# Kernel optimization log

Hardware: AMD Instinct MI355X
Metric: run time of the kernel (lower is better)

## Reference

```python
import jax, jax.numpy as jnp
import numpy as np

B, S, DM, H = 2, 4096, 512, 8
DEPTH = DM // H


def setup_inputs() -> dict:
    key = jax.random.key(0)
    ks = jax.random.split(key, 12)
    scale = 1.0 / np.sqrt(DM)
    return {
        "q": jax.random.normal(ks[0], (B, S, DM), jnp.float32),
        "k": jax.random.normal(ks[1], (B, S, DM), jnp.float32),
        "v": jax.random.normal(ks[2], (B, S, DM), jnp.float32),
        # padding-style mask: 1.0 = masked position, 0.0 = attend
        "mask": jax.random.bernoulli(ks[3], 0.1, (B, 1, 1, S)).astype(jnp.float32),
        "Wq": jax.random.normal(ks[4], (DM, DM), jnp.float32) * scale,
        "bq": jnp.zeros((DM,), jnp.float32),
        "Wk": jax.random.normal(ks[5], (DM, DM), jnp.float32) * scale,
        "bk": jnp.zeros((DM,), jnp.float32),
        "Wv": jax.random.normal(ks[6], (DM, DM), jnp.float32) * scale,
        "bv": jnp.zeros((DM,), jnp.float32),
        "Wo": jax.random.normal(ks[7], (DM, DM), jnp.float32) * scale,
        "bo": jnp.zeros((DM,), jnp.float32),
    }


def _split_heads(x):
    # [B, S, DM] -> [B, H, S, DEPTH]
    b, s, _ = x.shape
    return x.reshape(b, s, H, DEPTH).transpose(0, 2, 1, 3)


def reference(q, k, v, mask, Wq, bq, Wk, bk, Wv, bv, Wo, bo):
    qh = _split_heads(q @ Wq + bq)   # [B,H,S,D]
    kh = _split_heads(k @ Wk + bk)
    vh = _split_heads(v @ Wv + bv)
    logits = jnp.einsum("bhqd,bhkd->bhqk", qh, kh) / jnp.sqrt(
        jnp.asarray(DEPTH, qh.dtype))
    logits = logits + mask * (-1e9)
    attn = jax.nn.softmax(logits, axis=-1)          # [B,H,Sq,Sk]
    out = jnp.einsum("bhqk,bhkd->bhqd", attn, vh)   # [B,H,S,D]
    out = out.transpose(0, 2, 1, 3).reshape(q.shape[0], -1, DM)
    return out @ Wo + bo
```

## Files before the change

kernel.cpp:

```cpp
#include <hip/hip_runtime.h>
#include <math.h>

#define BDIM 2
#define SDIM 4096
#define DMODEL 512
#define NHEAD 8
#define DHEAD 64
#define MROWS (BDIM * SDIM)

typedef __attribute__((ext_vector_type(8))) short short8;
typedef __attribute__((ext_vector_type(4))) float f32x4;
typedef __attribute__((ext_vector_type(4))) int i32x4;

union S8I4 {
  short8 s;
  i32x4 i;
};

#define MFMA16(a, b, c) __builtin_amdgcn_mfma_f32_16x16x32_bf16((a), (b), (c), 0, 0, 0)
#define EXP2F(x) __builtin_amdgcn_exp2f(x)

#define SCALE2 0.18033688011112042f
#define MASKMUL -1.442695040e9f
#define M0C 16.0f

#define GLOAD_LDS16(g, l)                                                     \
  __builtin_amdgcn_global_load_lds(                                           \
      (const __attribute__((address_space(1))) void*)(g),                     \
      (__attribute__((address_space(3))) void*)(l), 16, 0, 0)

__device__ inline void bf16_split(float x, short& h, short& l) {
  unsigned u = __float_as_uint(x);
  h = (short)(u >> 16);
  float hf = __uint_as_float(u & 0xffff0000u);
  l = (short)(__float_as_uint(x - hf) >> 16);
}

__device__ inline int2 bf16_split_pack(float x0, float x1) {
  const unsigned u0 = __float_as_uint(x0), u1 = __float_as_uint(x1);
  const float d0 = x0 - __uint_as_float(u0 & 0xffff0000u);
  const float d1 = x1 - __uint_as_float(u1 & 0xffff0000u);
  int2 r;
  r.x = __builtin_amdgcn_perm(u1, u0, 0x07060302);
  r.y = __builtin_amdgcn_perm(__float_as_uint(d1), __float_as_uint(d0),
                              0x07060302);
  return r;
}

__global__ __launch_bounds__(256) void wsplit_kernel(
    const float* __restrict__ W0, const float* __restrict__ W1,
    const float* __restrict__ W2, const float* __restrict__ W3,
    short* __restrict__ T0h, short* __restrict__ T0l, short* __restrict__ T1h,
    short* __restrict__ T1l, short* __restrict__ T2h, short* __restrict__ T2l,
    short* __restrict__ T3h, short* __restrict__ T3l) {
  __shared__ short Th[64 * 72], Tl[64 * 72];
  const int tid = threadIdx.x;
  const int k0 = blockIdx.x * 64;
  const int n0 = blockIdx.y * 64;
  const int z = blockIdx.z;
  const float* W = (z == 0) ? W0 : (z == 1) ? W1 : (z == 2) ? W2 : W3;
  short* Oh = (z == 0) ? T0h : (z == 1) ? T1h : (z == 2) ? T2h : T3h;
  short* Ol = (z == 0) ? T0l : (z == 1) ? T1l : (z == 2) ? T2l : T3l;

  {
    const int r = tid >> 2;
    const int c16 = (tid & 3) * 16;
    short8 h0, h1, l0, l1;
#pragma unroll
    for (int g = 0; g < 2; g++) {
      const f32x4 a = *(const f32x4*)(W + (size_t)(k0 + r) * DMODEL + n0 + c16 + g * 8);
      const f32x4 b = *(const f32x4*)(W + (size_t)(k0 + r) * DMODEL + n0 + c16 + g * 8 + 4);
      short8& hh = g ? h1 : h0;
      short8& ll = g ? l1 : l0;
#pragma unroll
      for (int j = 0; j < 4; j++) {
        short x, y;
        bf16_split(a[j], x, y);
        hh[j] = x;
        ll[j] = y;
        bf16_split(b[j], x, y);
        hh[4 + j] = x;
        ll[4 + j] = y;
      }
    }
    *(short8*)&Th[r * 72 + c16] = h0;
    *(short8*)&Th[r * 72 + c16 + 8] = h1;
    *(short8*)&Tl[r * 72 + c16] = l0;
    *(short8*)&Tl[r * 72 + c16 + 8] = l1;
  }
  __syncthreads();
  {
    const int n = tid >> 2;
    const int kc = (tid & 3) * 16;
    short8 h0, h1, l0, l1;
#pragma unroll
    for (int i = 0; i < 8; i++) {
      h0[i] = Th[(kc + i) * 72 + n];
      h1[i] = Th[(kc + 8 + i) * 72 + n];
      l0[i] = Tl[(kc + i) * 72 + n];
      l1[i] = Tl[(kc + 8 + i) * 72 + n];
    }
    short* dh = Oh + (size_t)(n0 + n) * DMODEL + k0 + kc;
    short* dl = Ol + (size_t)(n0 + n) * DMODEL + k0 + kc;
    *(short8*)dh = h0;
    *(short8*)(dh + 8) = h1;
    *(short8*)dl = l0;
    *(short8*)(dl + 8) = l1;
  }
}

__global__ __launch_bounds__(512, 4) void proj4_kernel(
    const int mode_sel, const float* __restrict__ X0,
    const float* __restrict__ X1, const float* __restrict__ X2,
    const short* __restrict__ Wth0, const short* __restrict__ Wth1,
    const short* __restrict__ Wth2, const short* __restrict__ Wtl0,
    const short* __restrict__ Wtl1, const short* __restrict__ Wtl2,
    const float* __restrict__ bias0, const float* __restrict__ bias1,
    const float* __restrict__ bias2, float* __restrict__ out,
    short* __restrict__ qoh, short* __restrict__ qol, short* __restrict__ koh,
    short* __restrict__ kol, short* __restrict__ vth, short* __restrict__ vtl) {
  __shared__ short L[2 * 20480];
  const int tid = threadIdx.x;
  const int lane = tid & 63;
  const int w = tid >> 6;
  const int lane15 = lane & 15;
  const int quad = lane >> 4;
  const int m0 = blockIdx.x * 64;
  const int n0 = blockIdx.y * 256;
  const int z = blockIdx.z;
  const int mode = (mode_sel >= 0) ? mode_sel : (z == 2 ? 2 : 1);
  const float* X = (z == 0) ? X0 : (z == 1) ? X1 : X2;
  const short* Wth = (z == 0) ? Wth0 : (z == 1) ? Wth1 : Wth2;
  const short* Wtl = (z == 0) ? Wtl0 : (z == 1) ? Wtl1 : Wtl2;
  const float* bias = (z == 0) ? bias0 : (z == 1) ? bias1 : bias2;
  short* oh = (z == 0) ? qoh : koh;
  short* ol = (z == 0) ? qol : kol;
  const int wm = (w >> 2) * 32;
  const int wn = (w & 3) * 64;

  const char* gp[5];
  int stepb[5], ldso[5];
#pragma unroll
  for (int i = 0; i < 5; i++) {
    const int idx = w * 5 + i;
    if (idx < 8) {
      const int g = idx * 64 + lane;
      const int row = g >> 3, cs = g & 7;
      gp[i] = (const char*)(X + (size_t)(m0 + row) * DMODEL +
                            ((cs ^ (row & 7)) * 4));
      stepb[i] = 128;
    } else {
      const int gg = idx * 64 + lane - 512;
      const short* src = (gg < 1024) ? Wth : Wtl;
      const int a = gg & 1023;
      const int row = a >> 2, cs = a & 3;
      gp[i] = (const char*)(src + (size_t)(n0 + row) * DMODEL +
                            (cs ^ ((row >> 1) & 3)) * 8);
      stepb[i] = 64;
    }
    ldso[i] = idx * 512;
  }

  f32x4 c[2][4];
#pragma unroll
  for (int mt = 0; mt < 2; mt++)
#pragma unroll
    for (int nt = 0; nt < 4; nt++) c[mt][nt] = (f32x4){0.f, 0.f, 0.f, 0.f};

  constexpr int NT = DMODEL / 32;

#pragma unroll
  for (int i = 0; i < 5; i++) GLOAD_LDS16(gp[i], &L[ldso[i]]);

  for (int t = 0; t < NT; t++) {
    __syncthreads();
    if (t + 1 < NT) {
      short* dst = &L[((t + 1) & 1) * 20480];
#pragma unroll
      for (int i = 0; i < 5; i++)
        GLOAD_LDS16(gp[i] + (t + 1) * stepb[i], dst + ldso[i]);
    }
    const short* buf = &L[(t & 1) * 20480];
    const float* Af = (const float*)buf;
    short8 ah[2], al[2], bh[4], bl[4];
#pragma unroll
    for (int mt = 0; mt < 2; mt++) {
      const int r = wm + mt * 16 + lane15;
      const int c0 = ((quad * 2) ^ (r & 7)) * 4;
      const int c1 = ((quad * 2 + 1) ^ (r & 7)) * 4;
      const f32x4 a0 = *(const f32x4*)&Af[r * 32 + c0];
      const f32x4 a1 = *(const f32x4*)&Af[r * 32 + c1];
      S8I4 hh, ll;
      const int2 p0 = bf16_split_pack(a0[0], a0[1]);
      const int2 p1 = bf16_split_pack(a0[2], a0[3]);
      const int2 p2 = bf16_split_pack(a1[0], a1[1]);
      const int2 p3 = bf16_split_pack(a1[2], a1[3]);
      hh.i[0] = p0.x; ll.i[0] = p0.y;
      hh.i[1] = p1.x; ll.i[1] = p1.y;
      hh.i[2] = p2.x; ll.i[2] = p2.y;
      hh.i[3] = p3.x; ll.i[3] = p3.y;
      ah[mt] = hh.s;
      al[mt] = ll.s;
    }
#pragma unroll
    for (int nt = 0; nt < 4; nt++) {
      const int r = wn + nt * 16 + lane15;
      const int cb = (quad ^ ((r >> 1) & 3)) * 8;
      bh[nt] = *(const short8*)&buf[4096 + r * 32 + cb];
      bl[nt] = *(const short8*)&buf[12288 + r * 32 + cb];
    }
    __builtin_amdgcn_s_setprio(1);
#pragma unroll
    for (int mt = 0; mt < 2; mt++)
#pragma unroll
      for (int nt = 0; nt < 4; nt++) {
        c[mt][nt] = MFMA16(ah[mt], bh[nt], c[mt][nt]);
        c[mt][nt] = MFMA16(ah[mt], bl[nt], c[mt][nt]);
        c[mt][nt] = MFMA16(al[mt], bh[nt], c[mt][nt]);
      }
    __builtin_amdgcn_s_setprio(0);
  }

  if (mode == 2) {
    __syncthreads();
    short* Lh = L;
    short* Ll = L + 18432;
#pragma unroll
    for (int nt = 0; nt < 4; nt++) {
      const int n = wn + nt * 16 + lane15;
      const float bb = bias[n0 + n];
#pragma unroll
      for (int mt = 0; mt < 2; mt++)
#pragma unroll
        for (int r = 0; r < 4; r++) {
          const int m = wm + mt * 16 + quad * 4 + r;
          short x, y;
          bf16_split(c[mt][nt][r] + bb, x, y);
          Lh[n * 72 + m] = x;
          Ll[n * 72 + m] = y;
        }
    }
    __syncthreads();
    const int row = tid >> 1;
    const int half = tid & 1;
    const int n = n0 + row;
    const int hh = n >> 6, d = n & 63;
    const int bidx = m0 >> 12, s0 = m0 & 4095;
    const size_t tbase = ((size_t)(bidx * NHEAD + hh)) * SDIM * DHEAD +
                         (size_t)d * SDIM + s0 + half * 32;
#pragma unroll
    for (int i = 0; i < 4; i++) {
      *(short8*)(vth + tbase + i * 8) = *(const short8*)&Lh[row * 72 + half * 32 + i * 8];
      *(short8*)(vtl + tbase + i * 8) = *(const short8*)&Ll[row * 72 + half * 32 + i * 8];
    }
    return;
  }

#pragma unroll
  for (int nt = 0; nt < 4; nt++) {
    const int n = n0 + wn + nt * 16 + lane15;
    const float bb = bias[n];
#pragma unroll
    for (int mt = 0; mt < 2; mt++)
#pragma unroll
      for (int r = 0; r < 4; r++) {
        const int m = m0 + wm + mt * 16 + quad * 4 + r;
        const float val = c[mt][nt][r] + bb;
        if (mode == 1) {
          const int bidx = m >> 12;
          const int s = m & 4095;
          const int hh = n >> 6;
          const int d = n & 63;
          const size_t off =
              ((size_t)(bidx * NHEAD + hh) * SDIM + s) * DHEAD + d;
          short x, y;
          bf16_split(val, x, y);
          oh[off] = x;
          ol[off] = y;
        } else {
          out[(size_t)m * DMODEL + n] = val;
        }
      }
  }
}

#define KP 72
#define VP 72
#define PP 68

__global__ __launch_bounds__(256, 2) void flash_attn_kernel(
    const short* __restrict__ qhh, const short* __restrict__ qhl,
    const short* __restrict__ khh, const short* __restrict__ khl,
    const short* __restrict__ vth, const short* __restrict__ vtl,
    const float* __restrict__ mask, float* __restrict__ ctx) {
  __shared__ short Ksh[64 * KP], Ksl[64 * KP];
  __shared__ short Vsh[64 * VP], Vsl[64 * VP];
  __shared__ float Ps[128 * PP];

  const int tid = threadIdx.x;
  const int lane = tid & 63;
  const int w = tid >> 6;
  const int lane15 = lane & 15;
  const int quad = lane >> 4;

  const int bid = blockIdx.x + 32 * (blockIdx.y + NHEAD * blockIdx.z);
  const int sw = (bid & 7) * 64 + (bid >> 3);
  const int q0 = (sw & 31) * 128;
  const int h = (sw >> 5) & 7;
  const int b = sw >> 8;

  const size_t base = (size_t)(b * NHEAD + h) * SDIM * DHEAD;
  const short* Qh = qhh + base;
  const short* Ql = qhl + base;
  const short* Kh = khh + base;
  const short* Kl = khl + base;
  const short* Vh = vth + base;
  const short* Vl = vtl + base;
  const float* mb = mask + (size_t)b * SDIM;

  short8 qfh[2][2], qfl[2][2];
#pragma unroll
  for (int mt = 0; mt < 2; mt++) {
    const size_t row = q0 + w * 32 + mt * 16 + lane15;
#pragma unroll
    for (int ks = 0; ks < 2; ks++) {
      qfh[mt][ks] = *(const short8*)(Qh + row * DHEAD + ks * 32 + quad * 8);
      qfl[mt][ks] = *(const short8*)(Ql + row * DHEAD + ks * 32 + quad * 8);
    }
  }

  f32x4 o[2][4];
#pragma unroll
  for (int mt = 0; mt < 2; mt++)
#pragma unroll
    for (int dt = 0; dt < 4; dt++) o[mt][dt] = (f32x4){0.f, 0.f, 0.f, 0.f};
  float lr[2][4];
#pragma unroll
  for (int mt = 0; mt < 2; mt++)
#pragma unroll
    for (int r = 0; r < 4; r++) lr[mt][r] = 0.f;

  short8 onesb;
#pragma unroll
  for (int j = 0; j < 8; j++) onesb[j] = (short)0x3F80;

  const int sr = tid >> 2;
  const int sc = (tid & 3) * 16;

  short8 rg[8];
  rg[0] = *(const short8*)(Kh + (size_t)sr * DHEAD + sc);
  rg[1] = *(const short8*)(Kh + (size_t)sr * DHEAD + sc + 8);
  rg[2] = *(const short8*)(Kl + (size_t)sr * DHEAD + sc);
  rg[3] = *(const short8*)(Kl + (size_t)sr * DHEAD + sc + 8);
  rg[4] = *(const short8*)(Vh + (size_t)sr * SDIM + sc);
  rg[5] = *(const short8*)(Vh + (size_t)sr * SDIM + sc + 8);
  rg[6] = *(const short8*)(Vl + (size_t)sr * SDIM + sc);
  rg[7] = *(const short8*)(Vl + (size_t)sr * SDIM + sc + 8);

  for (int kt = 0; kt < SDIM / 64; kt++) {
    const int k0 = kt * 64;
    __builtin_amdgcn_s_barrier();
    __builtin_amdgcn_sched_barrier(0);
    *(short8*)&Ksh[sr * KP + sc] = rg[0];
    *(short8*)&Ksh[sr * KP + sc + 8] = rg[1];
    *(short8*)&Ksl[sr * KP + sc] = rg[2];
    *(short8*)&Ksl[sr * KP + sc + 8] = rg[3];
    *(short8*)&Vsh[sr * VP + sc] = rg[4];
    *(short8*)&Vsh[sr * VP + sc + 8] = rg[5];
    *(short8*)&Vsl[sr * VP + sc] = rg[6];
    *(short8*)&Vsl[sr * VP + sc + 8] = rg[7];
    if (kt + 1 < SDIM / 64) {
      const int k1 = k0 + 64;
      rg[0] = *(const short8*)(Kh + (size_t)(k1 + sr) * DHEAD + sc);
      rg[1] = *(const short8*)(Kh + (size_t)(k1 + sr) * DHEAD + sc + 8);
      rg[2] = *(const short8*)(Kl + (size_t)(k1 + sr) * DHEAD + sc);
      rg[3] = *(const short8*)(Kl + (size_t)(k1 + sr) * DHEAD + sc + 8);
      rg[4] = *(const short8*)(Vh + (size_t)sr * SDIM + k1 + sc);
      rg[5] = *(const short8*)(Vh + (size_t)sr * SDIM + k1 + sc + 8);
      rg[6] = *(const short8*)(Vl + (size_t)sr * SDIM + k1 + sc);
      rg[7] = *(const short8*)(Vl + (size_t)sr * SDIM + k1 + sc + 8);
    }
    float mv[4];
#pragma unroll
    for (int nt = 0; nt < 4; nt++)
      mv[nt] = fmaf(mb[k0 + nt * 16 + lane15], MASKMUL, -M0C);
    asm volatile("s_waitcnt lgkmcnt(0)" ::: "memory");
    __builtin_amdgcn_s_barrier();
    __builtin_amdgcn_sched_barrier(0);

    __builtin_amdgcn_s_setprio(1);
#pragma unroll
    for (int nt = 0; nt < 4; nt++) {
      short8 kbh[2], kbl[2];
#pragma unroll
      for (int ks = 0; ks < 2; ks++) {
        const int koff = (nt * 16 + lane15) * KP + ks * 32 + quad * 8;
        kbh[ks] = *(const short8*)&Ksh[koff];
        kbl[ks] = *(const short8*)&Ksl[koff];
      }
#pragma unroll
      for (int mt = 0; mt < 2; mt++) {
        f32x4 acc = (f32x4){0.f, 0.f, 0.f, 0.f};
#pragma unroll
        for (int ks = 0; ks < 2; ks++) {
          acc = MFMA16(qfh[mt][ks], kbh[ks], acc);
          acc = MFMA16(qfh[mt][ks], kbl[ks], acc);
          acc = MFMA16(qfl[mt][ks], kbh[ks], acc);
        }
#pragma unroll
        for (int r = 0; r < 4; r++) {
          const float p = EXP2F(fmaf(acc[r], SCALE2, mv[nt]));
          Ps[(w * 32 + mt * 16 + quad * 4 + r) * PP + nt * 16 + lane15] = p;
        }
      }
    }
    __builtin_amdgcn_s_setprio(0);

    short8 pah[2][2], pal[2][2];
#pragma unroll
    for (int mt = 0; mt < 2; mt++)
#pragma unroll
      for (int kf = 0; kf < 2; kf++) {
        const float* pr =
            &Ps[(w * 32 + mt * 16 + lane15) * PP + kf * 32 + quad * 8];
        const f32x4 p0 = *(const f32x4*)pr;
        const f32x4 p1 = *(const f32x4*)(pr + 4);
        S8I4 ph, pl;
        const int2 r0 = bf16_split_pack(p0[0], p0[1]);
        const int2 r1 = bf16_split_pack(p0[2], p0[3]);
        const int2 r2 = bf16_split_pack(p1[0], p1[1]);
        const int2 r3 = bf16_split_pack(p1[2], p1[3]);
        ph.i[0] = r0.x; pl.i[0] = r0.y;
        ph.i[1] = r1.x; pl.i[1] = r1.y;
        ph.i[2] = r2.x; pl.i[2] = r2.y;
        ph.i[3] = r3.x; pl.i[3] = r3.y;
        pah[mt][kf] = ph.s;
        pal[mt][kf] = pl.s;
      }

    __builtin_amdgcn_s_setprio(1);
#pragma unroll
    for (int mt = 0; mt < 2; mt++) {
      f32x4 racc = (f32x4){0.f, 0.f, 0.f, 0.f};
#pragma unroll
      for (int kf = 0; kf < 2; kf++) {
        racc = MFMA16(pah[mt][kf], onesb, racc);
        racc = MFMA16(pal[mt][kf], onesb, racc);
      }
#pragma unroll
      for (int r = 0; r < 4; r++) lr[mt][r] += racc[r];
    }

#pragma unroll
    for (int dt = 0; dt < 4; dt++)
#pragma unroll
      for (int kf = 0; kf < 2; kf++) {
        const int voff = (dt * 16 + lane15) * VP + kf * 32 + quad * 8;
        const short8 vbh = *(const short8*)&Vsh[voff];
        const short8 vbl = *(const short8*)&Vsl[voff];
#pragma unroll
        for (int mt = 0; mt < 2; mt++) {
          o[mt][dt] = MFMA16(pah[mt][kf], vbh, o[mt][dt]);
          o[mt][dt] = MFMA16(pah[mt][kf], vbl, o[mt][dt]);
          o[mt][dt] = MFMA16(pal[mt][kf], vbh, o[mt][dt]);
        }
      }
    __builtin_amdgcn_s_setprio(0);
  }

  float inv[2][4];
#pragma unroll
  for (int mt = 0; mt < 2; mt++)
#pragma unroll
    for (int r = 0; r < 4; r++) inv[mt][r] = 1.f / lr[mt][r];
#pragma unroll
  for (int mt = 0; mt < 2; mt++)
#pragma unroll
    for (int dt = 0; dt < 4; dt++)
#pragma unroll
      for (int r = 0; r < 4; r++) {
        const int q = q0 + w * 32 + mt * 16 + quad * 4 + r;
        const int col = h * DHEAD + dt * 16 + lane15;
        ctx[((size_t)b * SDIM + q) * DMODEL + col] = o[mt][dt][r] * inv[mt][r];
      }
}

extern "C" void kernel_launch(void* const* d_in, const int* in_sizes, int n_in,
                              void* d_out, int out_size, void* d_ws,
                              size_t ws_size, hipStream_t stream) {
  const float* q = (const float*)d_in[0];
  const float* k = (const float*)d_in[1];
  const float* v = (const float*)d_in[2];
  const float* mask = (const float*)d_in[3];
  const float* Wq = (const float*)d_in[4];
  const float* bq = (const float*)d_in[5];
  const float* Wk = (const float*)d_in[6];
  const float* bk = (const float*)d_in[7];
  const float* Wv = (const float*)d_in[8];
  const float* bv = (const float*)d_in[9];
  const float* Wo = (const float*)d_in[10];
  const float* bo = (const float*)d_in[11];
  float* out = (float*)d_out;

  char* W = (char*)d_ws;
  const size_t SZB = (size_t)MROWS * DMODEL * sizeof(short);
  short* q_h = (short*)(W + 0 * SZB);
  short* q_l = (short*)(W + 1 * SZB);
  short* k_h = (short*)(W + 2 * SZB);
  short* k_l = (short*)(W + 3 * SZB);
  short* vt_h = (short*)(W + 4 * SZB);
  short* vt_l = (short*)(W + 5 * SZB);
  float* ctx = (float*)(W + 6 * SZB);
  const size_t WSZ = (size_t)DMODEL * DMODEL * sizeof(short);
  char* WT = W + 8 * SZB;
  short* wtq_h = (short*)(WT + 0 * WSZ);
  short* wtq_l = (short*)(WT + 1 * WSZ);
  short* wtk_h = (short*)(WT + 2 * WSZ);
  short* wtk_l = (short*)(WT + 3 * WSZ);
  short* wtv_h = (short*)(WT + 4 * WSZ);
  short* wtv_l = (short*)(WT + 5 * WSZ);
  short* wto_h = (short*)(WT + 6 * WSZ);
  short* wto_l = (short*)(WT + 7 * WSZ);

  wsplit_kernel<<<dim3(DMODEL / 64, DMODEL / 64, 4), 256, 0, stream>>>(
      Wq, Wk, Wv, Wo, wtq_h, wtq_l, wtk_h, wtk_l, wtv_h, wtv_l, wto_h, wto_l);

  proj4_kernel<<<dim3(MROWS / 64, DMODEL / 256, 3), 512, 0, stream>>>(
      -1, q, k, v, wtq_h, wtk_h, wtv_h, wtq_l, wtk_l, wtv_l, bq, bk, bv,
      nullptr, q_h, q_l, k_h, k_l, vt_h, vt_l);

  flash_attn_kernel<<<dim3(SDIM / 128, NHEAD, BDIM), 256, 0, stream>>>(
      q_h, q_l, k_h, k_l, vt_h, vt_l, mask, ctx);

  proj4_kernel<<<dim3(MROWS / 64, DMODEL / 256, 1), 512, 0, stream>>>(
      0, ctx, nullptr, nullptr, wto_h, nullptr, nullptr, wto_l, nullptr,
      nullptr, bo, nullptr, nullptr, out, nullptr, nullptr, nullptr, nullptr,
      nullptr, nullptr);
}
```

Baseline: 377.3 us.

## Shrink projection tiles and stage loads through registers with single LDS buffer

```diff
diff --git a/kernel.cpp b/kernel.cpp
--- a/kernel.cpp
+++ b/kernel.cpp
@@ -23,11 +23,6 @@
 #define SCALE2 0.18033688011112042f
 #define MASKMUL -1.442695040e9f
 #define M0C 16.0f
-
-#define GLOAD_LDS16(g, l)                                                     \
-  __builtin_amdgcn_global_load_lds(                                           \
-      (const __attribute__((address_space(1))) void*)(g),                     \
-      (__attribute__((address_space(3))) void*)(l), 16, 0, 0)
 
 __device__ inline void bf16_split(float x, short& h, short& l) {
   unsigned u = __float_as_uint(x);
@@ -109,7 +104,7 @@
   }
 }
 
-__global__ __launch_bounds__(512, 4) void proj4_kernel(
+__global__ __launch_bounds__(256, 2) void proj5_kernel(
     const int mode_sel, const float* __restrict__ X0,
     const float* __restrict__ X1, const float* __restrict__ X2,
     const short* __restrict__ Wth0, const short* __restrict__ Wth1,
@@ -119,14 +114,14 @@
     const float* __restrict__ bias2, float* __restrict__ out,
     short* __restrict__ qoh, short* __restrict__ qol, short* __restrict__ koh,
     short* __restrict__ kol, short* __restrict__ vth, short* __restrict__ vtl) {
-  __shared__ short L[2 * 20480];
+  __shared__ short L[18432];
   const int tid = threadIdx.x;
   const int lane = tid & 63;
   const int w = tid >> 6;
   const int lane15 = lane & 15;
   const int quad = lane >> 4;
   const int m0 = blockIdx.x * 64;
-  const int n0 = blockIdx.y * 256;
+  const int n0 = blockIdx.y * 128;
   const int z = blockIdx.z;
   const int mode = (mode_sel >= 0) ? mode_sel : (z == 2 ? 2 : 1);
   const float* X = (z == 0) ? X0 : (z == 1) ? X1 : X2;
@@ -135,31 +130,25 @@
   const float* bias = (z == 0) ? bias0 : (z == 1) ? bias1 : bias2;
   short* oh = (z == 0) ? qoh : koh;
   short* ol = (z == 0) ? qol : kol;
-  const int wm = (w >> 2) * 32;
-  const int wn = (w & 3) * 64;
-
-  const char* gp[5];
-  int stepb[5], ldso[5];
-#pragma unroll
-  for (int i = 0; i < 5; i++) {
-    const int idx = w * 5 + i;
-    if (idx < 8) {
-      const int g = idx * 64 + lane;
-      const int row = g >> 3, cs = g & 7;
-      gp[i] = (const char*)(X + (size_t)(m0 + row) * DMODEL +
-                            ((cs ^ (row & 7)) * 4));
-      stepb[i] = 128;
-    } else {
-      const int gg = idx * 64 + lane - 512;
-      const short* src = (gg < 1024) ? Wth : Wtl;
-      const int a = gg & 1023;
-      const int row = a >> 2, cs = a & 3;
-      gp[i] = (const char*)(src + (size_t)(n0 + row) * DMODEL +
-                            (cs ^ ((row >> 1) & 3)) * 8);
-      stepb[i] = 64;
-    }
-    ldso[i] = idx * 512;
-  }
+  const int wm = (w >> 1) * 32;
+  const int wn = (w & 1) * 64;
+
+  const int rA0 = tid >> 3, csA = tid & 7;
+  const int rA1 = 32 + rA0;
+  const int rB0 = tid >> 2, csB = tid & 3;
+  const int rB1 = 64 + rB0;
+  const float* gA0 = X + (size_t)(m0 + rA0) * DMODEL + csA * 4;
+  const float* gA1 = X + (size_t)(m0 + rA1) * DMODEL + csA * 4;
+  const short* gB0 = Wth + (size_t)(n0 + rB0) * DMODEL + csB * 8;
+  const short* gB1 = Wth + (size_t)(n0 + rB1) * DMODEL + csB * 8;
+  const short* gB2 = Wtl + (size_t)(n0 + rB0) * DMODEL + csB * 8;
+  const short* gB3 = Wtl + (size_t)(n0 + rB1) * DMODEL + csB * 8;
+  const int oA0 = rA0 * 64 + ((csA ^ (rA0 & 7)) * 8);
+  const int oA1 = rA1 * 64 + ((csA ^ (rA1 & 7)) * 8);
+  const int oB0 = 4096 + rB0 * 32 + ((csB ^ ((rB0 >> 1) & 3)) * 8);
+  const int oB1 = 4096 + rB1 * 32 + ((csB ^ ((rB1 >> 1) & 3)) * 8);
+  const int oB2 = 4096 + oB0;
+  const int oB3 = 4096 + oB1;
 
   f32x4 c[2][4];
 #pragma unroll
@@ -169,19 +158,36 @@
 
   constexpr int NT = DMODEL / 32;
 
-#pragma unroll
-  for (int i = 0; i < 5; i++) GLOAD_LDS16(gp[i], &L[ldso[i]]);
+  short8 rg[6];
+  rg[0] = *(const short8*)gA0;
+  rg[1] = *(const short8*)gA1;
+  rg[2] = *(const short8*)gB0;
+  rg[3] = *(const short8*)gB1;
+  rg[4] = *(const short8*)gB2;
+  rg[5] = *(const short8*)gB3;
 
   for (int t = 0; t < NT; t++) {
-    __syncthreads();
+    __builtin_amdgcn_s_barrier();
+    __builtin_amdgcn_sched_barrier(0);
+    *(short8*)&L[oA0] = rg[0];
+    *(short8*)&L[oA1] = rg[1];
+    *(short8*)&L[oB0] = rg[2];
+    *(short8*)&L[oB1] = rg[3];
+    *(short8*)&L[oB2] = rg[4];
+    *(short8*)&L[oB3] = rg[5];
     if (t + 1 < NT) {
-      short* dst = &L[((t + 1) & 1) * 20480];
-#pragma unroll
-      for (int i = 0; i < 5; i++)
-        GLOAD_LDS16(gp[i] + (t + 1) * stepb[i], dst + ldso[i]);
-    }
-    const short* buf = &L[(t & 1) * 20480];
-    const float* Af = (const float*)buf;
+      rg[0] = *(const short8*)(gA0 + (t + 1) * 32);
+      rg[1] = *(const short8*)(gA1 + (t + 1) * 32);
+      rg[2] = *(const short8*)(gB0 + (t + 1) * 32);
+      rg[3] = *(const short8*)(gB1 + (t + 1) * 32);
+      rg[4] = *(const short8*)(gB2 + (t + 1) * 32);
+      rg[5] = *(const short8*)(gB3 + (t + 1) * 32);
+    }
+    asm volatile("s_waitcnt lgkmcnt(0)" ::: "memory");
+    __builtin_amdgcn_s_barrier();
+    __builtin_amdgcn_sched_barrier(0);
+
+    const float* Af = (const float*)L;
     short8 ah[2], al[2], bh[4], bl[4];
 #pragma unroll
     for (int mt = 0; mt < 2; mt++) {
@@ -204,10 +210,10 @@
     }
 #pragma unroll
     for (int nt = 0; nt < 4; nt++) {
-      const int r = wn + nt * 16 + lane15;
-      const int cb = (quad ^ ((r >> 1) & 3)) * 8;
-      bh[nt] = *(const short8*)&buf[4096 + r * 32 + cb];
-      bl[nt] = *(const short8*)&buf[12288 + r * 32 + cb];
+      const int rr = wn + nt * 16 + lane15;
+      const int cb = (quad ^ ((rr >> 1) & 3)) * 8;
+      bh[nt] = *(const short8*)&L[4096 + rr * 32 + cb];
+      bl[nt] = *(const short8*)&L[8192 + rr * 32 + cb];
     }
     __builtin_amdgcn_s_setprio(1);
 #pragma unroll
@@ -224,7 +230,7 @@
   if (mode == 2) {
     __syncthreads();
     short* Lh = L;
-    short* Ll = L + 18432;
+    short* Ll = L + 9216;
 #pragma unroll
     for (int nt = 0; nt < 4; nt++) {
       const int n = wn + nt * 16 + lane15;
@@ -250,8 +256,10 @@
                          (size_t)d * SDIM + s0 + half * 32;
 #pragma unroll
     for (int i = 0; i < 4; i++) {
-      *(short8*)(vth + tbase + i * 8) = *(const short8*)&Lh[row * 72 + half * 32 + i * 8];
-      *(short8*)(vtl + tbase + i * 8) = *(const short8*)&Ll[row * 72 + half * 32 + i * 8];
+      *(short8*)(vth + tbase + i * 8) =
+          *(const short8*)&Lh[row * 72 + half * 32 + i * 8];
+      *(short8*)(vtl + tbase + i * 8) =
+          *(const short8*)&Ll[row * 72 + half * 32 + i * 8];
     }
     return;
   }
@@ -525,14 +533,14 @@
   wsplit_kernel<<<dim3(DMODEL / 64, DMODEL / 64, 4), 256, 0, stream>>>(
       Wq, Wk, Wv, Wo, wtq_h, wtq_l, wtk_h, wtk_l, wtv_h, wtv_l, wto_h, wto_l);
 
-  proj4_kernel<<<dim3(MROWS / 64, DMODEL / 256, 3), 512, 0, stream>>>(
+  proj5_kernel<<<dim3(MROWS / 64, DMODEL / 128, 3), 256, 0, stream>>>(
       -1, q, k, v, wtq_h, wtk_h, wtv_h, wtq_l, wtk_l, wtv_l, bq, bk, bv,
       nullptr, q_h, q_l, k_h, k_l, vt_h, vt_l);
 
   flash_attn_kernel<<<dim3(SDIM / 128, NHEAD, BDIM), 256, 0, stream>>>(
       q_h, q_l, k_h, k_l, vt_h, vt_l, mask, ctx);
 
-  proj4_kernel<<<dim3(MROWS / 64, DMODEL / 256, 1), 512, 0, stream>>>(
+  proj5_kernel<<<dim3(MROWS / 64, DMODEL / 128, 1), 256, 0, stream>>>(
       0, ctx, nullptr, nullptr, wto_h, nullptr, nullptr, wto_l, nullptr,
       nullptr, bo, nullptr, nullptr, out, nullptr, nullptr, nullptr, nullptr,
       nullptr, nullptr);
```

After: 371.5 us. Within noise of the previous version (-1.5%).
